# Optimization experiments

Hardware: AMD Instinct MI355X
Metric: run time of the kernel (lower is better)

## Reference

```python
import jax, jax.numpy as jnp
import numpy as np

B, L, D_MODEL, D_FF, N_EXPERTS, TOP_K = 32, 256, 512, 2048, 8, 2
EPS = 1e-9


def setup_inputs() -> dict:
    key = jax.random.key(0)
    ks = jax.random.split(key, 7)
    scale1 = 1.0 / np.sqrt(D_MODEL)
    scale2 = 1.0 / np.sqrt(D_FF)
    return {
        "cycle_curve_data": jax.random.normal(ks[0], (B, L, D_MODEL), jnp.float32),
        "logits": jax.random.normal(ks[1], (B, N_EXPERTS), jnp.float32),
        "moe_masks": jax.random.randint(ks[2], (B, N_EXPERTS), 0, 2, jnp.int32),
        "W1": jax.random.normal(ks[3], (N_EXPERTS, D_MODEL, D_FF), jnp.float32) * scale1,
        "b1": jax.random.normal(ks[4], (N_EXPERTS, D_FF), jnp.float32) * scale1,
        "W2": jax.random.normal(ks[5], (N_EXPERTS, D_FF, D_MODEL), jnp.float32) * scale2,
        "b2": jax.random.normal(ks[6], (N_EXPERTS, D_MODEL), jnp.float32) * scale2,
    }


def _gates(logits, moe_masks):
    # softmax over experts, zero out unavailable experts, keep top-k, renormalize
    mask = (moe_masks == 1).astype(logits.dtype)               # [B, E]
    p = jax.nn.softmax(logits, axis=1) * mask                  # [B, E]
    _, idx = jax.lax.top_k(p, TOP_K)                           # [B, K]
    topk_mask = jnp.zeros_like(p).at[jnp.arange(p.shape[0])[:, None], idx].set(1.0)
    p = p * topk_mask
    return p / (jnp.sum(p, axis=1, keepdims=True) + EPS)       # [B, E]


def reference(cycle_curve_data, logits, moe_masks, W1, b1, W2, b2):
    gates = _gates(logits, moe_masks)                          # [B, E]
    x = cycle_curve_data                                       # [B, L, D]
    # dense equivalent of per-expert gather -> MLP -> gate-weighted scatter-combine
    h = jnp.einsum("bld,edf->eblf", x, W1) + b1[:, None, None, :]   # [E,B,L,F]
    h = jax.nn.gelu(h, approximate=False)
    out = jnp.einsum("be,eblf,efd->bld", gates, h, W2)
    out = out + jnp.einsum("be,ed->bd", gates, b2)[:, None, :]      # [B,L,D]
    return out
```

## Files before the change

### kernel.cpp

```cpp
#include <hip/hip_runtime.h>

#define B_SZ 32
#define L_SZ 256
#define D_SZ 512
#define F_SZ 2048
#define E_SZ 8
#define P_SZ 64
#define BK   32

typedef __attribute__((ext_vector_type(8))) short bf16x8;
typedef __attribute__((ext_vector_type(4))) float f32x4;

__device__ __forceinline__ unsigned short f2bf(float f) {
  unsigned int u = __builtin_bit_cast(unsigned int, f);
  u += 0x7fffu + ((u >> 16) & 1u);
  return (unsigned short)(u >> 16);
}

__device__ __forceinline__ void async16(const void* g, void* l) {
  __builtin_amdgcn_global_load_lds(
      (const __attribute__((address_space(1))) unsigned int*)g,
      (__attribute__((address_space(3))) unsigned int*)l, 16, 0, 0);
}

__device__ __forceinline__ float gelu_f(float x) {
  float a = fabsf(x) * 0.70710678118654752f;
  float t = __builtin_amdgcn_rcpf(1.0f + 0.3275911f * a);
  float y = t * (0.254829592f +
            t * (-0.284496736f +
            t * (1.421413741f +
            t * (-1.453152027f +
            t * 1.061405429f))));
  float e = __expf(-a * a);
  float erf_abs = 1.0f - y * e;
  float erf_v = (x < 0.f) ? -erf_abs : erf_abs;
  return 0.5f * x * (1.0f + erf_v);
}

#define PREP_CONV_BLKS 4096
#define PREP_TR_BLKS   2048
#define PREP_TOTAL     (1 + PREP_CONV_BLKS + 2 * PREP_TR_BLKS)

__global__ __launch_bounds__(256) void prep_kernel(
    const float* __restrict__ logits, const int* __restrict__ masks,
    const float* __restrict__ x,
    const float* __restrict__ W1, const float* __restrict__ W2,
    int* __restrict__ sel_e, float* __restrict__ sel_g,
    unsigned short* __restrict__ xb,
    unsigned short* __restrict__ w1t, unsigned short* __restrict__ w2t) {
  __shared__ float tile[64][65];
  int blk = blockIdx.x;
  int tid = threadIdx.x;

  if (blk == 0) {
    int b = tid;
    if (b >= B_SZ) return;
    float lg[E_SZ], p[E_SZ];
    float mx = -1e30f;
    for (int e = 0; e < E_SZ; ++e) { lg[e] = logits[b * E_SZ + e]; mx = fmaxf(mx, lg[e]); }
    float s = 0.f;
    for (int e = 0; e < E_SZ; ++e) { p[e] = expf(lg[e] - mx); s += p[e]; }
    for (int e = 0; e < E_SZ; ++e) p[e] = (masks[b * E_SZ + e] == 1) ? (p[e] / s) : 0.f;
    int i0 = 0, i1 = 1; float v0 = -1.f, v1 = -1.f;
    for (int e = 0; e < E_SZ; ++e) {
      float v = p[e];
      if (v > v0)      { v1 = v0; i1 = i0; v0 = v; i0 = e; }
      else if (v > v1) { v1 = v;  i1 = e; }
    }
    float den = v0 + v1 + 1e-9f;
    sel_e[2 * b] = i0;  sel_e[2 * b + 1] = i1;
    sel_g[2 * b] = v0 / den;
    sel_g[2 * b + 1] = v1 / den;
    return;
  }
  blk -= 1;

  if (blk < PREP_CONV_BLKS) {
    int i = blk * 256 + tid;
    float4 v = ((const float4*)x)[i];
    ushort4 o;
    o.x = f2bf(v.x); o.y = f2bf(v.y); o.z = f2bf(v.z); o.w = f2bf(v.w);
    ((ushort4*)xb)[i] = o;
    return;
  }
  blk -= PREP_CONV_BLKS;

  const float* in; unsigned short* out; int R, C, ls;
  if (blk < PREP_TR_BLKS) { in = W1; out = w1t; R = D_SZ; C = F_SZ; ls = 5; }
  else { blk -= PREP_TR_BLKS; in = W2; out = w2t; R = F_SZ; C = D_SZ; ls = 3; }
  int z = blk >> 8;
  int rem = blk & 255;
  int tr = rem >> ls, tc = rem & ((1 << ls) - 1);
  int r0 = tr * 64, c0 = tc * 64;
  const float* ip = in + (size_t)z * R * C;
  unsigned short* op = out + (size_t)z * C * R;
  int tx = tid & 63, ty = tid >> 6;
#pragma unroll
  for (int i = 0; i < 16; ++i) {
    int r = i * 4 + ty;
    tile[r][tx] = ip[(size_t)(r0 + r) * C + c0 + tx];
  }
  __syncthreads();
#pragma unroll
  for (int uu = 0; uu < 4; ++uu) {
    int u = uu * 256 + tid;
    int cc = u >> 4, q = u & 15;
    ushort4 o;
    o.x = f2bf(tile[q * 4 + 0][cc]);
    o.y = f2bf(tile[q * 4 + 1][cc]);
    o.z = f2bf(tile[q * 4 + 2][cc]);
    o.w = f2bf(tile[q * 4 + 3][cc]);
    *(ushort4*)(op + (size_t)(c0 + cc) * R + r0 + q * 4) = o;
  }
}

__global__ __launch_bounds__(256, 4) void moe_gemm1(
    const unsigned short* __restrict__ Xb,
    const unsigned short* __restrict__ W1t,
    const float* __restrict__ b1,
    const int* __restrict__ sel_e,
    unsigned short* __restrict__ H) {
  int p = blockIdx.z;
  int b = p >> 1;
  int e = sel_e[p];
  int f0 = blockIdx.x * 128;
  int l0 = blockIdx.y * 128;

  __shared__ __align__(16) unsigned short As[128 * BK];
  __shared__ __align__(16) unsigned short Bs[128 * BK];

  const unsigned short* Abase = Xb  + ((size_t)b * L_SZ + l0) * D_SZ;
  const unsigned short* Bbase = W1t + ((size_t)e * F_SZ + f0) * D_SZ;

  int tid = threadIdx.x;
  int lane = tid & 63;
  int w = tid >> 6, wm = w & 1, wn = w >> 1;
  int lrow = lane & 15, kg = lane >> 4;

  int seg0 = w * 128 + lane;
  int row0 = seg0 >> 2, ks0 = (seg0 & 3) * 8;
  int seg1 = seg0 + 64;
  int row1 = seg1 >> 2, ks1 = (seg1 & 3) * 8;

  f32x4 acc[4][4] = {};

  for (int k0 = 0; k0 < D_SZ; k0 += BK) {
    async16(Abase + (size_t)row0 * D_SZ + k0 + ks0, &As[seg0 * 8]);
    async16(Abase + (size_t)row1 * D_SZ + k0 + ks1, &As[seg1 * 8]);
    async16(Bbase + (size_t)row0 * D_SZ + k0 + ks0, &Bs[seg0 * 8]);
    async16(Bbase + (size_t)row1 * D_SZ + k0 + ks1, &Bs[seg1 * 8]);
    __syncthreads();
    bf16x8 af[4], bfr[4];
#pragma unroll
    for (int i = 0; i < 4; ++i)
      af[i] = *(const bf16x8*)&As[(wm * 64 + i * 16 + lrow) * BK + kg * 8];
#pragma unroll
    for (int j = 0; j < 4; ++j)
      bfr[j] = *(const bf16x8*)&Bs[(wn * 64 + j * 16 + lrow) * BK + kg * 8];
#pragma unroll
    for (int i = 0; i < 4; ++i)
#pragma unroll
      for (int j = 0; j < 4; ++j)
        acc[i][j] = __builtin_amdgcn_mfma_f32_16x16x32_bf16(af[i], bfr[j], acc[i][j], 0, 0, 0);
    __syncthreads();
  }

  unsigned short* Hp = H + ((size_t)p * L_SZ + l0) * F_SZ + f0;
  float b1v[4];
#pragma unroll
  for (int j = 0; j < 4; ++j)
    b1v[j] = b1[e * F_SZ + f0 + wn * 64 + j * 16 + lrow];
#pragma unroll
  for (int i = 0; i < 4; ++i) {
    int rbase = wm * 64 + i * 16 + kg * 4;
#pragma unroll
    for (int j = 0; j < 4; ++j) {
      int c = wn * 64 + j * 16 + lrow;
#pragma unroll
      for (int r = 0; r < 4; ++r) {
        float v = gelu_f(acc[i][j][r] + b1v[j]);
        Hp[(size_t)(rbase + r) * F_SZ + c] = f2bf(v);
      }
    }
  }
}

__global__ __launch_bounds__(256, 4) void moe_gemm2(
    const unsigned short* __restrict__ H,
    const unsigned short* __restrict__ W2t,
    const int* __restrict__ sel_e,
    const float* __restrict__ sel_g,
    float* __restrict__ part,
    float* __restrict__ Out) {
  int lin = blockIdx.x;
  int q   = lin & 7;
  int d   = (lin >> 3) & 3;
  int g8  = lin >> 5;
  int gg  = g8 * 8 + q;
  int p   = gg >> 1;
  int l0  = (gg & 1) * 128;
  int d0  = d * 128;
  int b   = p >> 1;
  int e   = sel_e[p];
  float g = sel_g[p];
  float* dst = (p & 1) ? Out : part;

  __shared__ __align__(16) unsigned short As[128 * BK];
  __shared__ __align__(16) unsigned short Bs[128 * BK];

  int tid = threadIdx.x;
  int lane = tid & 63;
  int w = tid >> 6, wm = w & 1, wn = w >> 1;
  int lrow = lane & 15, kg = lane >> 4;
  int seg0 = w * 128 + lane;
  int row0 = seg0 >> 2, ks0 = (seg0 & 3) * 8;
  int seg1 = seg0 + 64;
  int row1 = seg1 >> 2, ks1 = (seg1 & 3) * 8;

  const unsigned short* Abase = H   + ((size_t)p * L_SZ + l0) * F_SZ;
  const unsigned short* Bbase = W2t + ((size_t)e * D_SZ + d0) * F_SZ;

  f32x4 acc[4][4] = {};
  for (int k0 = 0; k0 < F_SZ; k0 += BK) {
    async16(Abase + (size_t)row0 * F_SZ + k0 + ks0, &As[seg0 * 8]);
    async16(Abase + (size_t)row1 * F_SZ + k0 + ks1, &As[seg1 * 8]);
    async16(Bbase + (size_t)row0 * F_SZ + k0 + ks0, &Bs[seg0 * 8]);
    async16(Bbase + (size_t)row1 * F_SZ + k0 + ks1, &Bs[seg1 * 8]);
    __syncthreads();
    bf16x8 af[4], bfr[4];
#pragma unroll
    for (int i = 0; i < 4; ++i)
      af[i] = *(const bf16x8*)&As[(wm * 64 + i * 16 + lrow) * BK + kg * 8];
#pragma unroll
    for (int j = 0; j < 4; ++j)
      bfr[j] = *(const bf16x8*)&Bs[(wn * 64 + j * 16 + lrow) * BK + kg * 8];
#pragma unroll
    for (int i = 0; i < 4; ++i)
#pragma unroll
      for (int j = 0; j < 4; ++j)
        acc[i][j] = __builtin_amdgcn_mfma_f32_16x16x32_bf16(af[i], bfr[j], acc[i][j], 0, 0, 0);
    __syncthreads();
  }

  float* Op = dst + ((size_t)b * L_SZ + l0) * D_SZ + d0;
#pragma unroll
  for (int i = 0; i < 4; ++i) {
    int rbase = wm * 64 + i * 16 + kg * 4;
#pragma unroll
    for (int j = 0; j < 4; ++j) {
      int c = wn * 64 + j * 16 + lrow;
#pragma unroll
      for (int r = 0; r < 4; ++r)
        Op[(size_t)(rbase + r) * D_SZ + c] = g * acc[i][j][r];
    }
  }
}

__global__ __launch_bounds__(256) void combine_kernel(
    const float* __restrict__ part, const float* __restrict__ b2,
    const int* __restrict__ sel_e, const float* __restrict__ sel_g,
    float* __restrict__ Out) {
  int i = blockIdx.x * 256 + threadIdx.x;
  int d4 = i & (D_SZ / 4 - 1);
  int b  = i >> 15;
  int e0 = sel_e[2 * b], e1 = sel_e[2 * b + 1];
  float g0 = sel_g[2 * b], g1 = sel_g[2 * b + 1];
  float4 pv = ((const float4*)part)[i];
  float4 o  = ((float4*)Out)[i];
  float4 v0 = ((const float4*)(b2 + (size_t)e0 * D_SZ))[d4];
  float4 v1 = ((const float4*)(b2 + (size_t)e1 * D_SZ))[d4];
  o.x += pv.x + g0 * v0.x + g1 * v1.x;
  o.y += pv.y + g0 * v0.y + g1 * v1.y;
  o.z += pv.z + g0 * v0.z + g1 * v1.z;
  o.w += pv.w + g0 * v0.w + g1 * v1.w;
  ((float4*)Out)[i] = o;
}

extern "C" void kernel_launch(void* const* d_in, const int* in_sizes, int n_in,
                              void* d_out, int out_size, void* d_ws, size_t ws_size,
                              hipStream_t stream) {
  const float* x      = (const float*)d_in[0];
  const float* logits = (const float*)d_in[1];
  const int*   masks  = (const int*)d_in[2];
  const float* W1     = (const float*)d_in[3];
  const float* b1     = (const float*)d_in[4];
  const float* W2     = (const float*)d_in[5];
  const float* b2     = (const float*)d_in[6];
  float* out = (float*)d_out;

  char* ws = (char*)d_ws;
  int*   sel_e = (int*)ws;
  float* sel_g = (float*)(ws + 256);
  unsigned short* xb  = (unsigned short*)(ws + 1024);
  unsigned short* w1t = xb  + (size_t)B_SZ * L_SZ * D_SZ;
  unsigned short* w2t = w1t + (size_t)E_SZ * F_SZ * D_SZ;
  unsigned short* Hbuf = w2t + (size_t)E_SZ * D_SZ * F_SZ;
  float* part = (float*)(ws + 1024);

  prep_kernel<<<PREP_TOTAL, 256, 0, stream>>>(logits, masks, x, W1, W2,
                                              sel_e, sel_g, xb, w1t, w2t);
  moe_gemm1<<<dim3(F_SZ / 128, L_SZ / 128, P_SZ), 256, 0, stream>>>(
      xb, w1t, b1, sel_e, Hbuf);
  moe_gemm2<<<512, 256, 0, stream>>>(Hbuf, w2t, sel_e, sel_g, part, out);
  combine_kernel<<<(B_SZ * L_SZ * D_SZ / 4) / 256, 256, 0, stream>>>(
      part, b2, sel_e, sel_g, out);
}
```

Before: 244.5 us.

## Load GEMM A operands directly to registers, widen K tile, stage epilogues through LDS

Both MoE GEMMs now read the activation operand straight from global memory into registers, so only the weight tile goes through LDS, and BK is doubled to 64 to halve the number of barriers per K sweep. GEMM1 gets an XCD-aware 1D block mapping so that blocks sharing an expert land on the same XCD. Both epilogues are staged through padded LDS so global stores are coalesced 16-byte writes. The b2 bias add moves from the combine kernel into the gemm2 epilogue, which leaves combine as a plain add. The direct-to-register A loads get no LDS reuse across waves and raise register pressure, which is why occupancy is lowered to 3.

After: 293.1 us. 19.9% more time.

```diff
diff --git a/kernel.cpp b/kernel.cpp
--- a/kernel.cpp
+++ b/kernel.cpp
@@ -6,7 +6,7 @@
 #define F_SZ 2048
 #define E_SZ 8
 #define P_SZ 64
-#define BK   32
+#define BK   64
 
 typedef __attribute__((ext_vector_type(8))) short bf16x8;
 typedef __attribute__((ext_vector_type(4))) float f32x4;
@@ -114,62 +114,80 @@
   }
 }
 
-__global__ __launch_bounds__(256, 4) void moe_gemm1(
+__global__ __launch_bounds__(256, 3) void moe_gemm1(
     const unsigned short* __restrict__ Xb,
     const unsigned short* __restrict__ W1t,
     const float* __restrict__ b1,
     const int* __restrict__ sel_e,
     unsigned short* __restrict__ H) {
-  int p = blockIdx.z;
-  int b = p >> 1;
-  int e = sel_e[p];
-  int f0 = blockIdx.x * 128;
-  int l0 = blockIdx.y * 128;
-
-  __shared__ __align__(16) unsigned short As[128 * BK];
-  __shared__ __align__(16) unsigned short Bs[128 * BK];
-
-  const unsigned short* Abase = Xb  + ((size_t)b * L_SZ + l0) * D_SZ;
-  const unsigned short* Bbase = W1t + ((size_t)e * F_SZ + f0) * D_SZ;
+  __shared__ __align__(16) char smem[33792];
+  unsigned short* Bs = (unsigned short*)smem;
+
+  int lin = blockIdx.x;
+  int xcd = lin & 7;
+  int f   = (lin >> 3) & 15;
+  int grp = lin >> 7;
+  int pl  = grp * 8 + xcd;
+  int p   = pl >> 1;
+  int l0  = (pl & 1) * 128;
+  int f0  = f * 128;
+  int b   = p >> 1;
+  int e   = sel_e[p];
 
   int tid = threadIdx.x;
   int lane = tid & 63;
   int w = tid >> 6, wm = w & 1, wn = w >> 1;
   int lrow = lane & 15, kg = lane >> 4;
 
-  int seg0 = w * 128 + lane;
-  int row0 = seg0 >> 2, ks0 = (seg0 & 3) * 8;
-  int seg1 = seg0 + 64;
-  int row1 = seg1 >> 2, ks1 = (seg1 & 3) * 8;
+  const unsigned short* Bbase = W1t + ((size_t)e * F_SZ + f0) * D_SZ;
+  const unsigned short* Arow[4];
+#pragma unroll
+  for (int i = 0; i < 4; ++i)
+    Arow[i] = Xb + ((size_t)b * L_SZ + l0 + wm * 64 + i * 16 + lrow) * D_SZ + kg * 8;
+
+  int srow[4], skof[4];
+#pragma unroll
+  for (int c = 0; c < 4; ++c) {
+    int seg = c * 256 + tid;
+    srow[c] = seg >> 3;
+    skof[c] = (seg & 7) * 8;
+  }
 
   f32x4 acc[4][4] = {};
 
   for (int k0 = 0; k0 < D_SZ; k0 += BK) {
-    async16(Abase + (size_t)row0 * D_SZ + k0 + ks0, &As[seg0 * 8]);
-    async16(Abase + (size_t)row1 * D_SZ + k0 + ks1, &As[seg1 * 8]);
-    async16(Bbase + (size_t)row0 * D_SZ + k0 + ks0, &Bs[seg0 * 8]);
-    async16(Bbase + (size_t)row1 * D_SZ + k0 + ks1, &Bs[seg1 * 8]);
-    __syncthreads();
-    bf16x8 af[4], bfr[4];
-#pragma unroll
-    for (int i = 0; i < 4; ++i)
-      af[i] = *(const bf16x8*)&As[(wm * 64 + i * 16 + lrow) * BK + kg * 8];
-#pragma unroll
-    for (int j = 0; j < 4; ++j)
-      bfr[j] = *(const bf16x8*)&Bs[(wn * 64 + j * 16 + lrow) * BK + kg * 8];
-#pragma unroll
-    for (int i = 0; i < 4; ++i)
+#pragma unroll
+    for (int c = 0; c < 4; ++c)
+      async16(Bbase + (size_t)srow[c] * D_SZ + k0 + skof[c],
+              Bs + (size_t)(c * 256 + tid) * 8);
+    bf16x8 a[2][4];
+#pragma unroll
+    for (int s = 0; s < 2; ++s)
+#pragma unroll
+      for (int i = 0; i < 4; ++i)
+        a[s][i] = *(const bf16x8*)(Arow[i] + k0 + s * 32);
+    __syncthreads();
+#pragma unroll
+    for (int s = 0; s < 2; ++s) {
+      bf16x8 bf[4];
 #pragma unroll
       for (int j = 0; j < 4; ++j)
-        acc[i][j] = __builtin_amdgcn_mfma_f32_16x16x32_bf16(af[i], bfr[j], acc[i][j], 0, 0, 0);
-    __syncthreads();
-  }
-
-  unsigned short* Hp = H + ((size_t)p * L_SZ + l0) * F_SZ + f0;
+        bf[j] = *(const bf16x8*)&Bs[(wn * 64 + j * 16 + lrow) * BK + s * 32 + kg * 8];
+#pragma unroll
+      for (int i = 0; i < 4; ++i)
+#pragma unroll
+        for (int j = 0; j < 4; ++j)
+          acc[i][j] = __builtin_amdgcn_mfma_f32_16x16x32_bf16(a[s][i], bf[j], acc[i][j], 0, 0, 0);
+    }
+    __syncthreads();
+  }
+
   float b1v[4];
 #pragma unroll
   for (int j = 0; j < 4; ++j)
     b1v[j] = b1[e * F_SZ + f0 + wn * 64 + j * 16 + lrow];
+
+  unsigned short* Ep = (unsigned short*)smem;
 #pragma unroll
   for (int i = 0; i < 4; ++i) {
     int rbase = wm * 64 + i * 16 + kg * 4;
@@ -177,102 +195,138 @@
     for (int j = 0; j < 4; ++j) {
       int c = wn * 64 + j * 16 + lrow;
 #pragma unroll
-      for (int r = 0; r < 4; ++r) {
-        float v = gelu_f(acc[i][j][r] + b1v[j]);
-        Hp[(size_t)(rbase + r) * F_SZ + c] = f2bf(v);
-      }
-    }
-  }
-}
-
-__global__ __launch_bounds__(256, 4) void moe_gemm2(
+      for (int r = 0; r < 4; ++r)
+        Ep[(rbase + r) * 132 + c] = f2bf(gelu_f(acc[i][j][r] + b1v[j]));
+    }
+  }
+  __syncthreads();
+  unsigned short* Hp = H + ((size_t)p * L_SZ + l0) * F_SZ + f0;
+#pragma unroll
+  for (int u = 0; u < 8; ++u) {
+    int row = u * 16 + (tid >> 4);
+    int colb = (tid & 15) * 8;
+    bf16x8 v = *(const bf16x8*)&Ep[row * 132 + colb];
+    *(bf16x8*)(Hp + (size_t)row * F_SZ + colb) = v;
+  }
+}
+
+__global__ __launch_bounds__(256, 3) void moe_gemm2(
     const unsigned short* __restrict__ H,
     const unsigned short* __restrict__ W2t,
+    const float* __restrict__ b2,
     const int* __restrict__ sel_e,
     const float* __restrict__ sel_g,
     float* __restrict__ part,
     float* __restrict__ Out) {
+  __shared__ __align__(16) char smem[33792];
+  unsigned short* Bs = (unsigned short*)smem;
+
   int lin = blockIdx.x;
-  int q   = lin & 7;
+  int xcd = lin & 7;
   int d   = (lin >> 3) & 3;
-  int g8  = lin >> 5;
-  int gg  = g8 * 8 + q;
-  int p   = gg >> 1;
-  int l0  = (gg & 1) * 128;
+  int grp = lin >> 5;
+  int pl  = grp * 8 + xcd;
+  int p   = pl >> 1;
+  int l0  = (pl & 1) * 128;
   int d0  = d * 128;
   int b   = p >> 1;
   int e   = sel_e[p];
   float g = sel_g[p];
-  float* dst = (p & 1) ? Out : part;
-
-  __shared__ __align__(16) unsigned short As[128 * BK];
-  __shared__ __align__(16) unsigned short Bs[128 * BK];
 
   int tid = threadIdx.x;
   int lane = tid & 63;
   int w = tid >> 6, wm = w & 1, wn = w >> 1;
   int lrow = lane & 15, kg = lane >> 4;
-  int seg0 = w * 128 + lane;
-  int row0 = seg0 >> 2, ks0 = (seg0 & 3) * 8;
-  int seg1 = seg0 + 64;
-  int row1 = seg1 >> 2, ks1 = (seg1 & 3) * 8;
-
-  const unsigned short* Abase = H   + ((size_t)p * L_SZ + l0) * F_SZ;
+
   const unsigned short* Bbase = W2t + ((size_t)e * D_SZ + d0) * F_SZ;
+  const unsigned short* Arow[4];
+#pragma unroll
+  for (int i = 0; i < 4; ++i)
+    Arow[i] = H + ((size_t)p * L_SZ + l0 + wm * 64 + i * 16 + lrow) * F_SZ + kg * 8;
+
+  int srow[4], skof[4];
+#pragma unroll
+  for (int c = 0; c < 4; ++c) {
+    int seg = c * 256 + tid;
+    srow[c] = seg >> 3;
+    skof[c] = (seg & 7) * 8;
+  }
 
   f32x4 acc[4][4] = {};
+
   for (int k0 = 0; k0 < F_SZ; k0 += BK) {
-    async16(Abase + (size_t)row0 * F_SZ + k0 + ks0, &As[seg0 * 8]);
-    async16(Abase + (size_t)row1 * F_SZ + k0 + ks1, &As[seg1 * 8]);
-    async16(Bbase + (size_t)row0 * F_SZ + k0 + ks0, &Bs[seg0 * 8]);
-    async16(Bbase + (size_t)row1 * F_SZ + k0 + ks1, &Bs[seg1 * 8]);
-    __syncthreads();
-    bf16x8 af[4], bfr[4];
-#pragma unroll
-    for (int i = 0; i < 4; ++i)
-      af[i] = *(const bf16x8*)&As[(wm * 64 + i * 16 + lrow) * BK + kg * 8];
-#pragma unroll
-    for (int j = 0; j < 4; ++j)
-      bfr[j] = *(const bf16x8*)&Bs[(wn * 64 + j * 16 + lrow) * BK + kg * 8];
-#pragma unroll
-    for (int i = 0; i < 4; ++i)
+#pragma unroll
+    for (int c = 0; c < 4; ++c)
+      async16(Bbase + (size_t)srow[c] * F_SZ + k0 + skof[c],
+              Bs + (size_t)(c * 256 + tid) * 8);
+    bf16x8 a[2][4];
+#pragma unroll
+    for (int s = 0; s < 2; ++s)
+#pragma unroll
+      for (int i = 0; i < 4; ++i)
+        a[s][i] = *(const bf16x8*)(Arow[i] + k0 + s * 32);
+    __syncthreads();
+#pragma unroll
+    for (int s = 0; s < 2; ++s) {
+      bf16x8 bf[4];
 #pragma unroll
       for (int j = 0; j < 4; ++j)
-        acc[i][j] = __builtin_amdgcn_mfma_f32_16x16x32_bf16(af[i], bfr[j], acc[i][j], 0, 0, 0);
-    __syncthreads();
-  }
-
+        bf[j] = *(const bf16x8*)&Bs[(wn * 64 + j * 16 + lrow) * BK + s * 32 + kg * 8];
+#pragma unroll
+      for (int i = 0; i < 4; ++i)
+#pragma unroll
+        for (int j = 0; j < 4; ++j)
+          acc[i][j] = __builtin_amdgcn_mfma_f32_16x16x32_bf16(a[s][i], bf[j], acc[i][j], 0, 0, 0);
+    }
+    __syncthreads();
+  }
+
+  float bias[4] = {0.f, 0.f, 0.f, 0.f};
+  if (p & 1) {
+    int e0 = sel_e[2 * b], e1 = sel_e[2 * b + 1];
+    float g0 = sel_g[2 * b], g1 = sel_g[2 * b + 1];
+#pragma unroll
+    for (int j = 0; j < 4; ++j) {
+      int dd = d0 + wn * 64 + j * 16 + lrow;
+      bias[j] = g0 * b2[e0 * D_SZ + dd] + g1 * b2[e1 * D_SZ + dd];
+    }
+  }
+  float* dst = (p & 1) ? Out : part;
   float* Op = dst + ((size_t)b * L_SZ + l0) * D_SZ + d0;
-#pragma unroll
-  for (int i = 0; i < 4; ++i) {
-    int rbase = wm * 64 + i * 16 + kg * 4;
-#pragma unroll
-    for (int j = 0; j < 4; ++j) {
-      int c = wn * 64 + j * 16 + lrow;
-#pragma unroll
-      for (int r = 0; r < 4; ++r)
-        Op[(size_t)(rbase + r) * D_SZ + c] = g * acc[i][j][r];
+  float* Ef = (float*)smem;
+#pragma unroll
+  for (int h = 0; h < 2; ++h) {
+    __syncthreads();
+    if (wm == h) {
+#pragma unroll
+      for (int i = 0; i < 4; ++i) {
+        int rl = i * 16 + kg * 4;
+#pragma unroll
+        for (int j = 0; j < 4; ++j) {
+          int c = wn * 64 + j * 16 + lrow;
+#pragma unroll
+          for (int r = 0; r < 4; ++r)
+            Ef[(rl + r) * 130 + c] = g * acc[i][j][r] + bias[j];
+        }
+      }
+    }
+    __syncthreads();
+#pragma unroll
+    for (int u = 0; u < 8; ++u) {
+      int rl = u * 8 + (tid >> 5);
+      int c4 = (tid & 31) * 4;
+      float4 v = *(const float4*)&Ef[rl * 130 + c4];
+      *(float4*)(Op + (size_t)(h * 64 + rl) * D_SZ + c4) = v;
     }
   }
 }
 
 __global__ __launch_bounds__(256) void combine_kernel(
-    const float* __restrict__ part, const float* __restrict__ b2,
-    const int* __restrict__ sel_e, const float* __restrict__ sel_g,
-    float* __restrict__ Out) {
+    const float* __restrict__ part, float* __restrict__ Out) {
   int i = blockIdx.x * 256 + threadIdx.x;
-  int d4 = i & (D_SZ / 4 - 1);
-  int b  = i >> 15;
-  int e0 = sel_e[2 * b], e1 = sel_e[2 * b + 1];
-  float g0 = sel_g[2 * b], g1 = sel_g[2 * b + 1];
   float4 pv = ((const float4*)part)[i];
   float4 o  = ((float4*)Out)[i];
-  float4 v0 = ((const float4*)(b2 + (size_t)e0 * D_SZ))[d4];
-  float4 v1 = ((const float4*)(b2 + (size_t)e1 * D_SZ))[d4];
-  o.x += pv.x + g0 * v0.x + g1 * v1.x;
-  o.y += pv.y + g0 * v0.y + g1 * v1.y;
-  o.z += pv.z + g0 * v0.z + g1 * v1.z;
-  o.w += pv.w + g0 * v0.w + g1 * v1.w;
+  o.x += pv.x; o.y += pv.y; o.z += pv.z; o.w += pv.w;
   ((float4*)Out)[i] = o;
 }
 
@@ -299,9 +353,7 @@
 
   prep_kernel<<<PREP_TOTAL, 256, 0, stream>>>(logits, masks, x, W1, W2,
                                               sel_e, sel_g, xb, w1t, w2t);
-  moe_gemm1<<<dim3(F_SZ / 128, L_SZ / 128, P_SZ), 256, 0, stream>>>(
-      xb, w1t, b1, sel_e, Hbuf);
-  moe_gemm2<<<512, 256, 0, stream>>>(Hbuf, w2t, sel_e, sel_g, part, out);
-  combine_kernel<<<(B_SZ * L_SZ * D_SZ / 4) / 256, 256, 0, stream>>>(
-      part, b2, sel_e, sel_g, out);
-}
+  moe_gemm1<<<2048, 256, 0, stream>>>(xb, w1t, b1, sel_e, Hbuf);
+  moe_gemm2<<<512, 256, 0, stream>>>(Hbuf, w2t, b2, sel_e, sel_g, part, out);
+  combine_kernel<<<(B_SZ * L_SZ * D_SZ / 4) / 256, 256, 0, stream>>>(part, out);
+}
```

## Switch GEMMs to 32x32 MFMA, deepen K step, remap gemm1 grid, fold bias

Applied to the files above, without the earlier changes.

Both expert GEMMs now use 32x32x16 bf16 MFMA tiles with a 2x2 accumulator per wave instead of 4x4 16x16 tiles. Each sync interval loads two 32-wide K slabs, which halves the number of barriers. gemm1 moves to a 1-D grid that assigns blocks to XCDs so blocks sharing a token slab group together for cache reuse. The b2 bias add moves from the combine kernel into gemm2's epilogue. The trade-off is more LDS per block and a more strided store pattern in the epilogue.

Result: no change. 245.5 us (+0.4%).

```diff
diff --git a/kernel.cpp b/kernel.cpp
--- a/kernel.cpp
+++ b/kernel.cpp
@@ -6,10 +6,10 @@
 #define F_SZ 2048
 #define E_SZ 8
 #define P_SZ 64
-#define BK   32
-
-typedef __attribute__((ext_vector_type(8))) short bf16x8;
-typedef __attribute__((ext_vector_type(4))) float f32x4;
+#define BK2  32
+
+typedef __attribute__((ext_vector_type(8)))  short bf16x8;
+typedef __attribute__((ext_vector_type(16))) float f32x16;
 
 __device__ __forceinline__ unsigned short f2bf(float f) {
   unsigned int u = __builtin_bit_cast(unsigned int, f);
@@ -120,78 +120,92 @@
     const float* __restrict__ b1,
     const int* __restrict__ sel_e,
     unsigned short* __restrict__ H) {
-  int p = blockIdx.z;
-  int b = p >> 1;
-  int e = sel_e[p];
-  int f0 = blockIdx.x * 128;
-  int l0 = blockIdx.y * 128;
-
-  __shared__ __align__(16) unsigned short As[128 * BK];
-  __shared__ __align__(16) unsigned short Bs[128 * BK];
-
-  const unsigned short* Abase = Xb  + ((size_t)b * L_SZ + l0) * D_SZ;
-  const unsigned short* Bbase = W1t + ((size_t)e * F_SZ + f0) * D_SZ;
+  __shared__ __align__(16) unsigned short As[2][128 * BK2];
+  __shared__ __align__(16) unsigned short Bs[2][128 * BK2];
+
+  int lin = blockIdx.x;
+  int xcd = lin & 7;
+  int f   = (lin >> 3) & 15;
+  int grp = lin >> 7;
+  int pl  = grp * 8 + xcd;
+  int p   = pl >> 1;
+  int l0  = (pl & 1) * 128;
+  int f0  = f * 128;
+  int b   = p >> 1;
+  int e   = sel_e[p];
 
   int tid = threadIdx.x;
   int lane = tid & 63;
   int w = tid >> 6, wm = w & 1, wn = w >> 1;
-  int lrow = lane & 15, kg = lane >> 4;
+  int m32 = lane & 31, kh = lane >> 5;
+
+  const unsigned short* Abase = Xb  + ((size_t)b * L_SZ + l0) * D_SZ;
+  const unsigned short* Bbase = W1t + ((size_t)e * F_SZ + f0) * D_SZ;
 
   int seg0 = w * 128 + lane;
   int row0 = seg0 >> 2, ks0 = (seg0 & 3) * 8;
   int seg1 = seg0 + 64;
   int row1 = seg1 >> 2, ks1 = (seg1 & 3) * 8;
 
-  f32x4 acc[4][4] = {};
-
-  for (int k0 = 0; k0 < D_SZ; k0 += BK) {
-    async16(Abase + (size_t)row0 * D_SZ + k0 + ks0, &As[seg0 * 8]);
-    async16(Abase + (size_t)row1 * D_SZ + k0 + ks1, &As[seg1 * 8]);
-    async16(Bbase + (size_t)row0 * D_SZ + k0 + ks0, &Bs[seg0 * 8]);
-    async16(Bbase + (size_t)row1 * D_SZ + k0 + ks1, &Bs[seg1 * 8]);
+  f32x16 acc[2][2] = {};
+
+  for (int k0 = 0; k0 < D_SZ; k0 += 2 * BK2) {
+#pragma unroll
+    for (int h = 0; h < 2; ++h) {
+      int kk = k0 + h * BK2;
+      async16(Abase + (size_t)row0 * D_SZ + kk + ks0, &As[h][seg0 * 8]);
+      async16(Abase + (size_t)row1 * D_SZ + kk + ks1, &As[h][seg1 * 8]);
+      async16(Bbase + (size_t)row0 * D_SZ + kk + ks0, &Bs[h][seg0 * 8]);
+      async16(Bbase + (size_t)row1 * D_SZ + kk + ks1, &Bs[h][seg1 * 8]);
+    }
     __syncthreads();
-    bf16x8 af[4], bfr[4];
-#pragma unroll
-    for (int i = 0; i < 4; ++i)
-      af[i] = *(const bf16x8*)&As[(wm * 64 + i * 16 + lrow) * BK + kg * 8];
-#pragma unroll
-    for (int j = 0; j < 4; ++j)
-      bfr[j] = *(const bf16x8*)&Bs[(wn * 64 + j * 16 + lrow) * BK + kg * 8];
-#pragma unroll
-    for (int i = 0; i < 4; ++i)
-#pragma unroll
-      for (int j = 0; j < 4; ++j)
-        acc[i][j] = __builtin_amdgcn_mfma_f32_16x16x32_bf16(af[i], bfr[j], acc[i][j], 0, 0, 0);
+#pragma unroll
+    for (int h = 0; h < 2; ++h)
+#pragma unroll
+      for (int s = 0; s < 2; ++s) {
+        int ko = s * 16 + kh * 8;
+        bf16x8 a0 = *(const bf16x8*)&As[h][(wm * 64 +      m32) * BK2 + ko];
+        bf16x8 a1 = *(const bf16x8*)&As[h][(wm * 64 + 32 + m32) * BK2 + ko];
+        bf16x8 b0 = *(const bf16x8*)&Bs[h][(wn * 64 +      m32) * BK2 + ko];
+        bf16x8 b1f = *(const bf16x8*)&Bs[h][(wn * 64 + 32 + m32) * BK2 + ko];
+        acc[0][0] = __builtin_amdgcn_mfma_f32_32x32x16_bf16(a0, b0,  acc[0][0], 0, 0, 0);
+        acc[0][1] = __builtin_amdgcn_mfma_f32_32x32x16_bf16(a0, b1f, acc[0][1], 0, 0, 0);
+        acc[1][0] = __builtin_amdgcn_mfma_f32_32x32x16_bf16(a1, b0,  acc[1][0], 0, 0, 0);
+        acc[1][1] = __builtin_amdgcn_mfma_f32_32x32x16_bf16(a1, b1f, acc[1][1], 0, 0, 0);
+      }
     __syncthreads();
   }
 
+  float b1v[2];
+#pragma unroll
+  for (int tj = 0; tj < 2; ++tj)
+    b1v[tj] = b1[e * F_SZ + f0 + wn * 64 + tj * 32 + m32];
+
   unsigned short* Hp = H + ((size_t)p * L_SZ + l0) * F_SZ + f0;
-  float b1v[4];
-#pragma unroll
-  for (int j = 0; j < 4; ++j)
-    b1v[j] = b1[e * F_SZ + f0 + wn * 64 + j * 16 + lrow];
-#pragma unroll
-  for (int i = 0; i < 4; ++i) {
-    int rbase = wm * 64 + i * 16 + kg * 4;
-#pragma unroll
-    for (int j = 0; j < 4; ++j) {
-      int c = wn * 64 + j * 16 + lrow;
-#pragma unroll
-      for (int r = 0; r < 4; ++r) {
-        float v = gelu_f(acc[i][j][r] + b1v[j]);
-        Hp[(size_t)(rbase + r) * F_SZ + c] = f2bf(v);
+#pragma unroll
+  for (int ti = 0; ti < 2; ++ti)
+#pragma unroll
+    for (int tj = 0; tj < 2; ++tj) {
+      int col = wn * 64 + tj * 32 + m32;
+#pragma unroll
+      for (int r = 0; r < 16; ++r) {
+        int row = wm * 64 + ti * 32 + (r & 3) + 8 * (r >> 2) + 4 * kh;
+        Hp[(size_t)row * F_SZ + col] = f2bf(gelu_f(acc[ti][tj][r] + b1v[tj]));
       }
     }
-  }
 }
 
 __global__ __launch_bounds__(256, 4) void moe_gemm2(
     const unsigned short* __restrict__ H,
     const unsigned short* __restrict__ W2t,
+    const float* __restrict__ b2,
     const int* __restrict__ sel_e,
     const float* __restrict__ sel_g,
     float* __restrict__ part,
     float* __restrict__ Out) {
+  __shared__ __align__(16) unsigned short As[2][128 * BK2];
+  __shared__ __align__(16) unsigned short Bs[2][128 * BK2];
+
   int lin = blockIdx.x;
   int q   = lin & 7;
   int d   = (lin >> 3) & 3;
@@ -203,76 +217,80 @@
   int b   = p >> 1;
   int e   = sel_e[p];
   float g = sel_g[p];
-  float* dst = (p & 1) ? Out : part;
-
-  __shared__ __align__(16) unsigned short As[128 * BK];
-  __shared__ __align__(16) unsigned short Bs[128 * BK];
 
   int tid = threadIdx.x;
   int lane = tid & 63;
   int w = tid >> 6, wm = w & 1, wn = w >> 1;
-  int lrow = lane & 15, kg = lane >> 4;
+  int m32 = lane & 31, kh = lane >> 5;
+
+  const unsigned short* Abase = H   + ((size_t)p * L_SZ + l0) * F_SZ;
+  const unsigned short* Bbase = W2t + ((size_t)e * D_SZ + d0) * F_SZ;
+
   int seg0 = w * 128 + lane;
   int row0 = seg0 >> 2, ks0 = (seg0 & 3) * 8;
   int seg1 = seg0 + 64;
   int row1 = seg1 >> 2, ks1 = (seg1 & 3) * 8;
 
-  const unsigned short* Abase = H   + ((size_t)p * L_SZ + l0) * F_SZ;
-  const unsigned short* Bbase = W2t + ((size_t)e * D_SZ + d0) * F_SZ;
-
-  f32x4 acc[4][4] = {};
-  for (int k0 = 0; k0 < F_SZ; k0 += BK) {
-    async16(Abase + (size_t)row0 * F_SZ + k0 + ks0, &As[seg0 * 8]);
-    async16(Abase + (size_t)row1 * F_SZ + k0 + ks1, &As[seg1 * 8]);
-    async16(Bbase + (size_t)row0 * F_SZ + k0 + ks0, &Bs[seg0 * 8]);
-    async16(Bbase + (size_t)row1 * F_SZ + k0 + ks1, &Bs[seg1 * 8]);
+  f32x16 acc[2][2] = {};
+
+  for (int k0 = 0; k0 < F_SZ; k0 += 2 * BK2) {
+#pragma unroll
+    for (int h = 0; h < 2; ++h) {
+      int kk = k0 + h * BK2;
+      async16(Abase + (size_t)row0 * F_SZ + kk + ks0, &As[h][seg0 * 8]);
+      async16(Abase + (size_t)row1 * F_SZ + kk + ks1, &As[h][seg1 * 8]);
+      async16(Bbase + (size_t)row0 * F_SZ + kk + ks0, &Bs[h][seg0 * 8]);
+      async16(Bbase + (size_t)row1 * F_SZ + kk + ks1, &Bs[h][seg1 * 8]);
+    }
     __syncthreads();
-    bf16x8 af[4], bfr[4];
-#pragma unroll
-    for (int i = 0; i < 4; ++i)
-      af[i] = *(const bf16x8*)&As[(wm * 64 + i * 16 + lrow) * BK + kg * 8];
-#pragma unroll
-    for (int j = 0; j < 4; ++j)
-      bfr[j] = *(const bf16x8*)&Bs[(wn * 64 + j * 16 + lrow) * BK + kg * 8];
-#pragma unroll
-    for (int i = 0; i < 4; ++i)
-#pragma unroll
-      for (int j = 0; j < 4; ++j)
-        acc[i][j] = __builtin_amdgcn_mfma_f32_16x16x32_bf16(af[i], bfr[j], acc[i][j], 0, 0, 0);
+#pragma unroll
+    for (int h = 0; h < 2; ++h)
+#pragma unroll
+      for (int s = 0; s < 2; ++s) {
+        int ko = s * 16 + kh * 8;
+        bf16x8 a0 = *(const bf16x8*)&As[h][(wm * 64 +      m32) * BK2 + ko];
+        bf16x8 a1 = *(const bf16x8*)&As[h][(wm * 64 + 32 + m32) * BK2 + ko];
+        bf16x8 b0 = *(const bf16x8*)&Bs[h][(wn * 64 +      m32) * BK2 + ko];
+        bf16x8 b1f = *(const bf16x8*)&Bs[h][(wn * 64 + 32 + m32) * BK2 + ko];
+        acc[0][0] = __builtin_amdgcn_mfma_f32_32x32x16_bf16(a0, b0,  acc[0][0], 0, 0, 0);
+        acc[0][1] = __builtin_amdgcn_mfma_f32_32x32x16_bf16(a0, b1f, acc[0][1], 0, 0, 0);
+        acc[1][0] = __builtin_amdgcn_mfma_f32_32x32x16_bf16(a1, b0,  acc[1][0], 0, 0, 0);
+        acc[1][1] = __builtin_amdgcn_mfma_f32_32x32x16_bf16(a1, b1f, acc[1][1], 0, 0, 0);
+      }
     __syncthreads();
   }
 
+  float bias[2] = {0.f, 0.f};
+  if (p & 1) {
+    int e0 = sel_e[2 * b], e1 = sel_e[2 * b + 1];
+    float g0 = sel_g[2 * b], g1 = sel_g[2 * b + 1];
+#pragma unroll
+    for (int tj = 0; tj < 2; ++tj) {
+      int dd = d0 + wn * 64 + tj * 32 + m32;
+      bias[tj] = g0 * b2[e0 * D_SZ + dd] + g1 * b2[e1 * D_SZ + dd];
+    }
+  }
+  float* dst = (p & 1) ? Out : part;
   float* Op = dst + ((size_t)b * L_SZ + l0) * D_SZ + d0;
 #pragma unroll
-  for (int i = 0; i < 4; ++i) {
-    int rbase = wm * 64 + i * 16 + kg * 4;
-#pragma unroll
-    for (int j = 0; j < 4; ++j) {
-      int c = wn * 64 + j * 16 + lrow;
-#pragma unroll
-      for (int r = 0; r < 4; ++r)
-        Op[(size_t)(rbase + r) * D_SZ + c] = g * acc[i][j][r];
-    }
-  }
+  for (int ti = 0; ti < 2; ++ti)
+#pragma unroll
+    for (int tj = 0; tj < 2; ++tj) {
+      int col = wn * 64 + tj * 32 + m32;
+#pragma unroll
+      for (int r = 0; r < 16; ++r) {
+        int row = wm * 64 + ti * 32 + (r & 3) + 8 * (r >> 2) + 4 * kh;
+        Op[(size_t)row * D_SZ + col] = g * acc[ti][tj][r] + bias[tj];
+      }
+    }
 }
 
 __global__ __launch_bounds__(256) void combine_kernel(
-    const float* __restrict__ part, const float* __restrict__ b2,
-    const int* __restrict__ sel_e, const float* __restrict__ sel_g,
-    float* __restrict__ Out) {
+    const float* __restrict__ part, float* __restrict__ Out) {
   int i = blockIdx.x * 256 + threadIdx.x;
-  int d4 = i & (D_SZ / 4 - 1);
-  int b  = i >> 15;
-  int e0 = sel_e[2 * b], e1 = sel_e[2 * b + 1];
-  float g0 = sel_g[2 * b], g1 = sel_g[2 * b + 1];
   float4 pv = ((const float4*)part)[i];
   float4 o  = ((float4*)Out)[i];
-  float4 v0 = ((const float4*)(b2 + (size_t)e0 * D_SZ))[d4];
-  float4 v1 = ((const float4*)(b2 + (size_t)e1 * D_SZ))[d4];
-  o.x += pv.x + g0 * v0.x + g1 * v1.x;
-  o.y += pv.y + g0 * v0.y + g1 * v1.y;
-  o.z += pv.z + g0 * v0.z + g1 * v1.z;
-  o.w += pv.w + g0 * v0.w + g1 * v1.w;
+  o.x += pv.x; o.y += pv.y; o.z += pv.z; o.w += pv.w;
   ((float4*)Out)[i] = o;
 }
 
@@ -299,9 +317,7 @@
 
   prep_kernel<<<PREP_TOTAL, 256, 0, stream>>>(logits, masks, x, W1, W2,
                                               sel_e, sel_g, xb, w1t, w2t);
-  moe_gemm1<<<dim3(F_SZ / 128, L_SZ / 128, P_SZ), 256, 0, stream>>>(
-      xb, w1t, b1, sel_e, Hbuf);
-  moe_gemm2<<<512, 256, 0, stream>>>(Hbuf, w2t, sel_e, sel_g, part, out);
-  combine_kernel<<<(B_SZ * L_SZ * D_SZ / 4) / 256, 256, 0, stream>>>(
-      part, b2, sel_e, sel_g, out);
-}
+  moe_gemm1<<<2048, 256, 0, stream>>>(xb, w1t, b1, sel_e, Hbuf);
+  moe_gemm2<<<512, 256, 0, stream>>>(Hbuf, w2t, b2, sel_e, sel_g, part, out);
+  combine_kernel<<<(B_SZ * L_SZ * D_SZ / 4) / 256, 256, 0, stream>>>(part, out);
+}
```
